# Optimization experiments

Measured on AMD Instinct MI355X. Metric: run time of the kernel, lower is better.

Reference implementation:

```python
import jax, jax.numpy as jnp
import numpy as np

B, CH, T = 8, 512, 1024
HEADS = 8
KC = CH // HEADS  # 64
BLOCK = 256       # block_length


def setup_inputs() -> dict:
    key = jax.random.key(0)
    ks = jax.random.split(key, 10)
    s = 0.05
    x = jax.random.normal(ks[0], (B, CH, T), jnp.float32)
    c = jax.random.normal(ks[1], (B, CH, T), jnp.float32)
    attn_mask = jnp.ones((1, 1, T, T), jnp.int32)
    # 1x1 Conv1d weights are just [out, in] matrices over the channel dim.
    Wq = jax.random.normal(ks[2], (CH, CH), jnp.float32) * s
    bq = jax.random.normal(ks[3], (CH,), jnp.float32) * s
    Wk = jax.random.normal(ks[4], (CH, CH), jnp.float32) * s
    bk = jax.random.normal(ks[5], (CH,), jnp.float32) * s
    Wv = jax.random.normal(ks[6], (CH, CH), jnp.float32) * s
    bv = jax.random.normal(ks[7], (CH,), jnp.float32) * s
    Wo = jax.random.normal(ks[8], (CH, CH), jnp.float32) * s
    bo = jax.random.normal(ks[9], (CH,), jnp.float32) * s
    return {"x": x, "c": c, "attn_mask": attn_mask,
            "Wq": Wq, "bq": bq, "Wk": Wk, "bk": bk,
            "Wv": Wv, "bv": bv, "Wo": Wo, "bo": bo}


def _proj(W, b, z):
    # 1x1 Conv1d: [B,C,T] -> [B,O,T]
    return jnp.einsum('oc,bct->bot', W, z) + b[None, :, None]


def reference(x, c, attn_mask, Wq, bq, Wk, bk, Wv, bv, Wo, bo):
    q = _proj(Wq, bq, x)
    k = _proj(Wk, bk, c)
    v = _proj(Wv, bv, c)

    def split_heads(z):  # [B,C,T] -> [B,H,T,KC]
        return z.reshape(B, HEADS, KC, T).transpose(0, 1, 3, 2)

    qh, kh, vh = split_heads(q), split_heads(k), split_heads(v)

    scale = jnp.asarray(1.0 / np.sqrt(KC), qh.dtype)
    scores = jnp.einsum('bhtd,bhsd->bhts', qh * scale, kh)  # [B,H,T,T]

    r = jnp.arange(T)
    diff = jnp.abs(r[None, :] - r[:, None])  # |i - j|, [T,T]
    # proximal bias: -log(1 + |i-j|)
    scores = scores + (-jnp.log1p(diff.astype(scores.dtype)))[None, None]
    # attention mask: masked_fill(mask == 0, -1e4)
    scores = jnp.where(attn_mask == 0, jnp.asarray(-1e4, scores.dtype), scores)
    # block-length band mask: keep |i-j| <= BLOCK (triu(-BLOCK).tril(BLOCK))
    band = (diff <= BLOCK)[None, None]
    scores = jnp.where(band, scores, jnp.asarray(-1e4, scores.dtype))

    p_attn = jax.nn.softmax(scores, axis=-1)
    out = jnp.einsum('bhts,bhsd->bhtd', p_attn, vh)  # [B,H,T,KC]
    out = out.transpose(0, 1, 3, 2).reshape(B, CH, T)  # merge heads -> [B,C,T]
    return _proj(Wo, bo, out)
```

## Files before the change

### kernel.cpp

```cpp
#include <hip/hip_runtime.h>
#include <stdint.h>

typedef unsigned short u16;
typedef __attribute__((ext_vector_type(8))) __bf16 bf16x8;
typedef __attribute__((ext_vector_type(4))) float f32x4;

constexpr int B_ = 8, CH = 512, T = 1024, NH = 8, HD = 64, BAND = 256;

__device__ inline u16 f2b(float f) {
  union { float f; uint32_t u; } v; v.f = f;
  uint32_t r = (v.u + 0x7fffu + ((v.u >> 16) & 1u)) >> 16;
  return (u16)r;
}

__device__ inline f32x4 mfma16(bf16x8 a, bf16x8 b, f32x4 c) {
  return __builtin_amdgcn_mfma_f32_16x16x32_bf16(a, b, c, 0, 0, 0);
}

__device__ __forceinline__ void gld16(const void* g, void* l) {
  __builtin_amdgcn_global_load_lds((__attribute__((address_space(1))) void*)(g),
                                   (__attribute__((address_space(3))) void*)(l),
                                   16, 0, 0);
}

__device__ __forceinline__ float exp2_hw(float x) { return __builtin_amdgcn_exp2f(x); }

__global__ __launch_bounds__(256) void cvt_w(const float* __restrict__ wq, const float* __restrict__ wk,
                                             const float* __restrict__ wv, const float* __restrict__ wo,
                                             u16* __restrict__ out) {
  int idx = blockIdx.x * 256 + threadIdx.x;
  int w = idx >> 15;
  const float* src = (w == 0) ? wq : (w == 1) ? wk : (w == 2) ? wv : wo;
  int e = (idx & 32767) * 8;
  f32x4 a = *(const f32x4*)(src + e);
  f32x4 b = *(const f32x4*)(src + e + 4);
  union { u16 h[8]; bf16x8 v; } r;
  r.h[0] = f2b(a[0]); r.h[1] = f2b(a[1]); r.h[2] = f2b(a[2]); r.h[3] = f2b(a[3]);
  r.h[4] = f2b(b[0]); r.h[5] = f2b(b[1]); r.h[6] = f2b(b[2]); r.h[7] = f2b(b[3]);
  *(bf16x8*)(out + (w << 18) + e) = r.v;
}

__global__ __launch_bounds__(256) void tr_cvt(const float* __restrict__ x, const float* __restrict__ c,
                                              u16* __restrict__ xT, u16* __restrict__ cT) {
  __shared__ float tile[32][33];
  int z = blockIdx.z;
  const float* src = (z < B_) ? x : c;
  u16* dst = (z < B_) ? xT : cT;
  int b = (z < B_) ? z : z - B_;
  int t0 = blockIdx.x * 32, c0 = blockIdx.y * 32;
  int tx = threadIdx.x & 31, ty = threadIdx.x >> 5;
#pragma unroll
  for (int k = 0; k < 4; k++)
    tile[ty + 8 * k][tx] = src[(long)(b * CH + c0 + ty + 8 * k) * T + t0 + tx];
  __syncthreads();
#pragma unroll
  for (int k = 0; k < 4; k++)
    dst[(long)(b * T + t0 + ty + 8 * k) * CH + c0 + tx] = f2b(tile[tx][ty + 8 * k]);
}

template <int TN, typename OT>
__device__ __forceinline__ void gemm_core(const u16* __restrict__ Ab, int lda,
                                          const u16* __restrict__ Bb, int ldb,
                                          OT* __restrict__ Cb, int ldc,
                                          const float* __restrict__ bi, bool brow,
                                          int m0, int n0, int K, u16* smA, u16* smB) {
  int t = threadIdx.x, lane = t & 63, wave = t >> 6;
  int cl = lane & 15, quad = lane >> 4;
  int wm = wave >> 1, wn = wave & 1;
  int rr = t >> 3, gs = t & 7;
  constexpr int NW = TN / 32;
  f32x4 acc[4][NW] = {};
  for (int k0 = 0; k0 < K; k0 += 64) {
    __syncthreads();
#pragma unroll
    for (int j = 0; j < 4; j++) {
      int R = j * 32 + rr;
      int gc = (gs ^ (R & 7)) << 3;
      gld16(Ab + (long)(m0 + R) * lda + k0 + gc, (char*)smA + j * 4096 + wave * 1024);
      if (j < TN / 32)
        gld16(Bb + (long)(n0 + R) * ldb + k0 + gc, (char*)smB + j * 4096 + wave * 1024);
    }
    __syncthreads();
#pragma unroll
    for (int ks = 0; ks < 2; ks++) {
      int g2 = ((ks << 2) | quad) ^ (cl & 7);
      bf16x8 af[4], bb[NW];
#pragma unroll
      for (int i = 0; i < 4; i++)
        af[i] = *(const bf16x8*)&smA[(wm * 64 + i * 16 + cl) * 64 + g2 * 8];
#pragma unroll
      for (int i = 0; i < NW; i++)
        bb[i] = *(const bf16x8*)&smB[(wn * (TN / 2) + i * 16 + cl) * 64 + g2 * 8];
#pragma unroll
      for (int mi = 0; mi < 4; mi++)
#pragma unroll
        for (int ni = 0; ni < NW; ni++)
          acc[mi][ni] = mfma16(af[mi], bb[ni], acc[mi][ni]);
    }
  }
#pragma unroll
  for (int mi = 0; mi < 4; mi++) {
    int row = m0 + wm * 64 + mi * 16 + quad * 4;
#pragma unroll
    for (int ni = 0; ni < NW; ni++) {
      int col = n0 + wn * (TN / 2) + ni * 16 + cl;
#pragma unroll
      for (int r = 0; r < 4; r++) {
        float v = acc[mi][ni][r] + (brow ? bi[row + r] : bi[col]);
        if constexpr (sizeof(OT) == 2) Cb[(long)(row + r) * ldc + col] = f2b(v);
        else Cb[(long)(row + r) * ldc + col] = v;
      }
    }
  }
}

__global__ __launch_bounds__(256, 3) void gemm_qkv(const u16* __restrict__ xT, const u16* __restrict__ cT,
                                                   const u16* __restrict__ Wb,
                                                   u16* __restrict__ Qb, u16* __restrict__ Kb, u16* __restrict__ Vb,
                                                   const float* __restrict__ bq, const float* __restrict__ bk,
                                                   const float* __restrict__ bv) {
  __shared__ u16 smA[128 * 64], smB[128 * 64];
  const long TCH = (long)T * CH;
  int z = blockIdx.z, sec = z >> 3, zz = z & 7, bx = blockIdx.x;
  const u16 *Ab, *Bb; u16* Cb; const float* bi;
  int m0, n0, ldc; bool brow;
  if (sec == 0) {
    Ab = xT + zz * TCH; Bb = Wb;           Cb = Qb + zz * TCH;        bi = bq;
    m0 = (bx >> 2) * 128; n0 = (bx & 3) * 128; ldc = CH; brow = false;
  } else if (sec == 1) {
    Ab = cT + zz * TCH; Bb = Wb + 262144;  Cb = Kb + zz * TCH;        bi = bk;
    m0 = (bx >> 2) * 128; n0 = (bx & 3) * 128; ldc = CH; brow = false;
  } else {
    Ab = Wb + 2 * 262144; Bb = cT + zz * TCH; Cb = Vb + zz * (long)CH * T; bi = bv;
    m0 = (bx & 3) * 128; n0 = (bx >> 2) * 128; ldc = T; brow = true;
  }
  gemm_core<128, u16>(Ab, CH, Bb, CH, Cb, ldc, bi, brow, m0, n0, CH, smA, smB);
}

__global__ __launch_bounds__(256, 4) void gemm_o(const u16* __restrict__ Wo, const u16* __restrict__ AO,
                                                 float* __restrict__ out, const float* __restrict__ bo) {
  __shared__ u16 smA[128 * 64], smB[64 * 64];
  int z = blockIdx.z;
  gemm_core<64, float>(Wo, CH, AO + z * (long)T * CH, CH, out + z * (long)CH * T, T,
                       bo, true, blockIdx.y * 128, blockIdx.x * 64, CH, smA, smB);
}

__global__ __launch_bounds__(256, 3) void attn(const u16* __restrict__ Q, const u16* __restrict__ Kt,
                                               const u16* __restrict__ V, u16* __restrict__ AO) {
  __shared__ u16 sK[2][64 * 64];
  __shared__ u16 sV[2][64 * 64];
  __shared__ u16 sP[4][16 * 72];
  int lane = threadIdx.x & 63, wave = threadIdx.x >> 6;
  int cl = lane & 15, quad = lane >> 4;
  int bx = blockIdx.x;
  int xcd = bx & 7, ii = bx >> 3;
  int bh = xcd * 8 + (ii & 7);
  int qt = ii >> 3;
  int b = bh >> 3, h = bh & 7;
  int tq0 = qt * 64;
  int tqw = tq0 + wave * 16;
  const u16* qb = Q + ((long)(b * T + tqw + cl) * CH) + h * HD;
  bf16x8 qf0 = *(const bf16x8*)(qb + quad * 8);
  bf16x8 qf1 = *(const bf16x8*)(qb + 32 + quad * 8);
  f32x4 acc[4] = {};
  float lr[4] = {0.f, 0.f, 0.f, 0.f};
  float fir[4];
#pragma unroll
  for (int r = 0; r < 4; r++) fir[r] = (float)(tqw + quad * 4 + r);
  int lo = tq0 - BAND; if (lo < 0) lo = 0;
  int hi = tq0 + 64 + BAND; if (hi > T) hi = T;
  int nt = (hi - lo) >> 6;

  int rl = lane >> 3, cg = lane & 7;
  const u16* ksrc = Kt + (long)b * T * CH + h * HD;
  const u16* vsrc = V + ((long)(b * CH + h * HD) * T);

#define STAGE(buf, j0)                                                          \
  {                                                                             \
    _Pragma("unroll")                                                           \
    for (int i = 0; i < 2; i++) {                                               \
      int r = wave * 16 + i * 8 + rl;                                           \
      int s = ((r >> 5) << 5) + ((r >> 4) & 1) + ((r & 15) << 1);               \
      gld16(ksrc + (long)(j0 + s) * CH + ((cg ^ (r & 7)) << 3),                 \
            (char*)&sK[buf][(wave * 16 + i * 8) * 64]);                         \
      gld16(vsrc + (long)r * T + (j0) + ((cg ^ (r & 7)) << 3),                  \
            (char*)&sV[buf][(wave * 16 + i * 8) * 64]);                         \
    }                                                                           \
  }

  STAGE(0, lo)
  constexpr float C2 = 0.125f * 1.4426950408889634f;
  for (int it = 0; it < nt; it++) {
    int cur = it & 1;
    int j0 = lo + it * 64;
    __syncthreads();
    if (it + 1 < nt) STAGE(1 - cur, j0 + 64)
    f32x4 sg[2][2];
#pragma unroll
    for (int p = 0; p < 2; p++)
#pragma unroll
      for (int sub = 0; sub < 2; sub++) {
        const u16* kr = &sK[cur][(p * 32 + sub * 16 + cl) * 64];
        bf16x8 k0 = *(const bf16x8*)&kr[((quad ^ (cl & 7)) << 3)];
        bf16x8 k1 = *(const bf16x8*)&kr[(((4 | quad) ^ (cl & 7)) << 3)];
        f32x4 z = {0.f, 0.f, 0.f, 0.f};
        sg[p][sub] = mfma16(qf1, k1, mfma16(qf0, k0, z));
      }
#pragma unroll
    for (int p = 0; p < 2; p++) {
      float jb = (float)(j0 + p * 32 + 2 * cl);
#pragma unroll
      for (int r = 0; r < 4; r++) {
        float de = fabsf(fir[r] - jb);
        float dd = fabsf(fir[r] - jb - 1.f);
        float pe = exp2_hw(sg[p][0][r] * C2) * __builtin_amdgcn_rcpf(1.f + de);
        float po = exp2_hw(sg[p][1][r] * C2) * __builtin_amdgcn_rcpf(1.f + dd);
        pe = (de <= 256.f) ? pe : 0.f;
        po = (dd <= 256.f) ? po : 0.f;
        lr[r] += pe + po;
        uint32_t ue, uo;
        { union { float f; uint32_t u; } cv; cv.f = pe; ue = cv.u; cv.f = po; uo = cv.u; }
        uint32_t pk = ((uo + 0x8000u) & 0xffff0000u) | ((ue + 0x8000u) >> 16);
        *(uint32_t*)&sP[wave][(quad * 4 + r) * 72 + p * 32 + 2 * cl] = pk;
      }
    }
#pragma unroll
    for (int ks = 0; ks < 2; ks++) {
      bf16x8 pf = *(bf16x8*)&sP[wave][cl * 72 + ks * 32 + quad * 8];
#pragma unroll
      for (int dg = 0; dg < 4; dg++) {
        bf16x8 vf = *(const bf16x8*)&sV[cur][(dg * 16 + cl) * 64 +
                                             ((((ks << 2) | quad) ^ (cl & 7)) << 3)];
        acc[dg] = mfma16(pf, vf, acc[dg]);
      }
    }
  }
#undef STAGE
  float inv[4];
#pragma unroll
  for (int r = 0; r < 4; r++) {
    float s = lr[r];
    s += __shfl_xor(s, 1); s += __shfl_xor(s, 2);
    s += __shfl_xor(s, 4); s += __shfl_xor(s, 8);
    inv[r] = __builtin_amdgcn_rcpf(s);
  }
#pragma unroll
  for (int dg = 0; dg < 4; dg++)
#pragma unroll
    for (int r = 0; r < 4; r++)
      AO[((long)(b * T + tqw + quad * 4 + r) * CH) + h * HD + dg * 16 + cl] = f2b(acc[dg][r] * inv[r]);
}

extern "C" void kernel_launch(void* const* d_in, const int* in_sizes, int n_in,
                              void* d_out, int out_size, void* d_ws, size_t ws_size,
                              hipStream_t stream) {
  const float* x  = (const float*)d_in[0];
  const float* c  = (const float*)d_in[1];
  const float* Wq = (const float*)d_in[3];
  const float* bq = (const float*)d_in[4];
  const float* Wk = (const float*)d_in[5];
  const float* bk = (const float*)d_in[6];
  const float* Wv = (const float*)d_in[7];
  const float* bv = (const float*)d_in[8];
  const float* Wo = (const float*)d_in[9];
  const float* bo = (const float*)d_in[10];
  float* out = (float*)d_out;

  const long NT = (long)B_ * T * CH;
  u16* Wb = (u16*)d_ws;
  u16* xT = Wb + 4 * 262144;
  u16* cT = xT + NT;
  u16* Qb = cT + NT;
  u16* Kb = Qb + NT;
  u16* Vb = Kb + NT;
  u16* AO = xT;

  cvt_w<<<dim3(512), dim3(256), 0, stream>>>(Wq, Wk, Wv, Wo, Wb);
  tr_cvt<<<dim3(32, 16, 16), dim3(256), 0, stream>>>(x, c, xT, cT);
  gemm_qkv<<<dim3(32, 1, 24), dim3(256), 0, stream>>>(xT, cT, Wb, Qb, Kb, Vb, bq, bk, bv);
  attn<<<dim3(1024), dim3(256), 0, stream>>>(Qb, Kb, Vb, AO);
  gemm_o<<<dim3(16, 4, 8), dim3(256), 0, stream>>>(Wb + 3 * 262144, AO, out, bo);
}
```

Before: 153.1 us.

## Double-buffer GEMM LDS loads and process two query tiles per attention block

The shared GEMM core now keeps two LDS buffers so the next K-slice is fetched while the current one is multiplied, with launch bounds lowered to fit the larger shared memory. The attention kernel now has each wave handle two 16-row query groups (128 queries per block) against the same staged K/V tiles, which halves the grid and reuses each K/V load for twice the queries. The cost is more registers and LDS per block and lower occupancy. The band window per block also widens, so some tiles fall entirely outside the band for one of the query groups and are computed anyway.

```diff
diff --git a/kernel.cpp b/kernel.cpp
--- a/kernel.cpp
+++ b/kernel.cpp
@@ -70,27 +70,36 @@
   int rr = t >> 3, gs = t & 7;
   constexpr int NW = TN / 32;
   f32x4 acc[4][NW] = {};
-  for (int k0 = 0; k0 < K; k0 += 64) {
-    __syncthreads();
+  auto stage = [&](int buf, int k0) {
 #pragma unroll
     for (int j = 0; j < 4; j++) {
       int R = j * 32 + rr;
       int gc = (gs ^ (R & 7)) << 3;
-      gld16(Ab + (long)(m0 + R) * lda + k0 + gc, (char*)smA + j * 4096 + wave * 1024);
-      if (j < TN / 32)
-        gld16(Bb + (long)(n0 + R) * ldb + k0 + gc, (char*)smB + j * 4096 + wave * 1024);
-    }
+      gld16(Ab + (long)(m0 + R) * lda + k0 + gc,
+            (char*)(smA + buf * 128 * 64) + j * 4096 + wave * 1024);
+      if (j < NW)
+        gld16(Bb + (long)(n0 + R) * ldb + k0 + gc,
+              (char*)(smB + buf * TN * 64) + j * 4096 + wave * 1024);
+    }
+  };
+  stage(0, 0);
+  int nk = K >> 6;
+  for (int it = 0; it < nk; it++) {
+    int cur = it & 1;
     __syncthreads();
+    if (it + 1 < nk) stage(1 - cur, (it + 1) << 6);
+    const u16* bA = smA + cur * 128 * 64;
+    const u16* bB = smB + cur * TN * 64;
 #pragma unroll
     for (int ks = 0; ks < 2; ks++) {
       int g2 = ((ks << 2) | quad) ^ (cl & 7);
       bf16x8 af[4], bb[NW];
 #pragma unroll
       for (int i = 0; i < 4; i++)
-        af[i] = *(const bf16x8*)&smA[(wm * 64 + i * 16 + cl) * 64 + g2 * 8];
+        af[i] = *(const bf16x8*)&bA[(wm * 64 + i * 16 + cl) * 64 + g2 * 8];
 #pragma unroll
       for (int i = 0; i < NW; i++)
-        bb[i] = *(const bf16x8*)&smB[(wn * (TN / 2) + i * 16 + cl) * 64 + g2 * 8];
+        bb[i] = *(const bf16x8*)&bB[(wn * (TN / 2) + i * 16 + cl) * 64 + g2 * 8];
 #pragma unroll
       for (int mi = 0; mi < 4; mi++)
 #pragma unroll
@@ -114,12 +123,12 @@
   }
 }
 
-__global__ __launch_bounds__(256, 3) void gemm_qkv(const u16* __restrict__ xT, const u16* __restrict__ cT,
+__global__ __launch_bounds__(256, 2) void gemm_qkv(const u16* __restrict__ xT, const u16* __restrict__ cT,
                                                    const u16* __restrict__ Wb,
                                                    u16* __restrict__ Qb, u16* __restrict__ Kb, u16* __restrict__ Vb,
                                                    const float* __restrict__ bq, const float* __restrict__ bk,
                                                    const float* __restrict__ bv) {
-  __shared__ u16 smA[128 * 64], smB[128 * 64];
+  __shared__ u16 smA[2 * 128 * 64], smB[2 * 128 * 64];
   const long TCH = (long)T * CH;
   int z = blockIdx.z, sec = z >> 3, zz = z & 7, bx = blockIdx.x;
   const u16 *Ab, *Bb; u16* Cb; const float* bi;
@@ -137,9 +146,9 @@
   gemm_core<128, u16>(Ab, CH, Bb, CH, Cb, ldc, bi, brow, m0, n0, CH, smA, smB);
 }
 
-__global__ __launch_bounds__(256, 4) void gemm_o(const u16* __restrict__ Wo, const u16* __restrict__ AO,
+__global__ __launch_bounds__(256, 3) void gemm_o(const u16* __restrict__ Wo, const u16* __restrict__ AO,
                                                  float* __restrict__ out, const float* __restrict__ bo) {
-  __shared__ u16 smA[128 * 64], smB[64 * 64];
+  __shared__ u16 smA[2 * 128 * 64], smB[2 * 64 * 64];
   int z = blockIdx.z;
   gemm_core<64, float>(Wo, CH, AO + z * (long)T * CH, CH, out + z * (long)CH * T, T,
                        bo, true, blockIdx.y * 128, blockIdx.x * 64, CH, smA, smB);
@@ -149,7 +158,7 @@
                                                const u16* __restrict__ V, u16* __restrict__ AO) {
   __shared__ u16 sK[2][64 * 64];
   __shared__ u16 sV[2][64 * 64];
-  __shared__ u16 sP[4][16 * 72];
+  __shared__ u16 sP[4][32 * 72];
   int lane = threadIdx.x & 63, wave = threadIdx.x >> 6;
   int cl = lane & 15, quad = lane >> 4;
   int bx = blockIdx.x;
@@ -157,18 +166,24 @@
   int bh = xcd * 8 + (ii & 7);
   int qt = ii >> 3;
   int b = bh >> 3, h = bh & 7;
-  int tq0 = qt * 64;
+  int tq0 = qt * 128;
   int tqw = tq0 + wave * 16;
-  const u16* qb = Q + ((long)(b * T + tqw + cl) * CH) + h * HD;
-  bf16x8 qf0 = *(const bf16x8*)(qb + quad * 8);
-  bf16x8 qf1 = *(const bf16x8*)(qb + 32 + quad * 8);
-  f32x4 acc[4] = {};
-  float lr[4] = {0.f, 0.f, 0.f, 0.f};
-  float fir[4];
-#pragma unroll
-  for (int r = 0; r < 4; r++) fir[r] = (float)(tqw + quad * 4 + r);
+  const u16* qb0 = Q + ((long)(b * T + tqw + cl) * CH) + h * HD;
+  const u16* qb1 = qb0 + (long)64 * CH;
+  bf16x8 qf[2][2];
+  qf[0][0] = *(const bf16x8*)(qb0 + quad * 8);
+  qf[0][1] = *(const bf16x8*)(qb0 + 32 + quad * 8);
+  qf[1][0] = *(const bf16x8*)(qb1 + quad * 8);
+  qf[1][1] = *(const bf16x8*)(qb1 + 32 + quad * 8);
+  f32x4 acc[2][4] = {};
+  float lr[2][4] = {};
+  float fir[2][4];
+#pragma unroll
+  for (int qg = 0; qg < 2; qg++)
+#pragma unroll
+    for (int r = 0; r < 4; r++) fir[qg][r] = (float)(tqw + qg * 64 + quad * 4 + r);
   int lo = tq0 - BAND; if (lo < 0) lo = 0;
-  int hi = tq0 + 64 + BAND; if (hi > T) hi = T;
+  int hi = tq0 + 128 + BAND; if (hi > T) hi = T;
   int nt = (hi - lo) >> 6;
 
   int rl = lane >> 3, cg = lane & 7;
@@ -195,7 +210,7 @@
     int j0 = lo + it * 64;
     __syncthreads();
     if (it + 1 < nt) STAGE(1 - cur, j0 + 64)
-    f32x4 sg[2][2];
+    f32x4 sg[2][2][2];
 #pragma unroll
     for (int p = 0; p < 2; p++)
 #pragma unroll
@@ -204,51 +219,60 @@
         bf16x8 k0 = *(const bf16x8*)&kr[((quad ^ (cl & 7)) << 3)];
         bf16x8 k1 = *(const bf16x8*)&kr[(((4 | quad) ^ (cl & 7)) << 3)];
         f32x4 z = {0.f, 0.f, 0.f, 0.f};
-        sg[p][sub] = mfma16(qf1, k1, mfma16(qf0, k0, z));
+        sg[0][p][sub] = mfma16(qf[0][1], k1, mfma16(qf[0][0], k0, z));
+        sg[1][p][sub] = mfma16(qf[1][1], k1, mfma16(qf[1][0], k0, z));
       }
 #pragma unroll
-    for (int p = 0; p < 2; p++) {
-      float jb = (float)(j0 + p * 32 + 2 * cl);
-#pragma unroll
-      for (int r = 0; r < 4; r++) {
-        float de = fabsf(fir[r] - jb);
-        float dd = fabsf(fir[r] - jb - 1.f);
-        float pe = exp2_hw(sg[p][0][r] * C2) * __builtin_amdgcn_rcpf(1.f + de);
-        float po = exp2_hw(sg[p][1][r] * C2) * __builtin_amdgcn_rcpf(1.f + dd);
-        pe = (de <= 256.f) ? pe : 0.f;
-        po = (dd <= 256.f) ? po : 0.f;
-        lr[r] += pe + po;
-        uint32_t ue, uo;
-        { union { float f; uint32_t u; } cv; cv.f = pe; ue = cv.u; cv.f = po; uo = cv.u; }
-        uint32_t pk = ((uo + 0x8000u) & 0xffff0000u) | ((ue + 0x8000u) >> 16);
-        *(uint32_t*)&sP[wave][(quad * 4 + r) * 72 + p * 32 + 2 * cl] = pk;
+    for (int qg = 0; qg < 2; qg++)
+#pragma unroll
+      for (int p = 0; p < 2; p++) {
+        float jb = (float)(j0 + p * 32 + 2 * cl);
+#pragma unroll
+        for (int r = 0; r < 4; r++) {
+          float de = fabsf(fir[qg][r] - jb);
+          float dd = fabsf(fir[qg][r] - jb - 1.f);
+          float pe = exp2_hw(sg[qg][p][0][r] * C2) * __builtin_amdgcn_rcpf(1.f + de);
+          float po = exp2_hw(sg[qg][p][1][r] * C2) * __builtin_amdgcn_rcpf(1.f + dd);
+          pe = (de <= 256.f) ? pe : 0.f;
+          po = (dd <= 256.f) ? po : 0.f;
+          lr[qg][r] += pe + po;
+          uint32_t ue, uo;
+          { union { float f; uint32_t u; } cv; cv.f = pe; ue = cv.u; cv.f = po; uo = cv.u; }
+          uint32_t pk = ((uo + 0x8000u) & 0xffff0000u) | ((ue + 0x8000u) >> 16);
+          *(uint32_t*)&sP[wave][(qg * 16 + quad * 4 + r) * 72 + p * 32 + 2 * cl] = pk;
+        }
       }
-    }
 #pragma unroll
     for (int ks = 0; ks < 2; ks++) {
-      bf16x8 pf = *(bf16x8*)&sP[wave][cl * 72 + ks * 32 + quad * 8];
+      bf16x8 pf0 = *(bf16x8*)&sP[wave][cl * 72 + ks * 32 + quad * 8];
+      bf16x8 pf1 = *(bf16x8*)&sP[wave][(16 + cl) * 72 + ks * 32 + quad * 8];
 #pragma unroll
       for (int dg = 0; dg < 4; dg++) {
         bf16x8 vf = *(const bf16x8*)&sV[cur][(dg * 16 + cl) * 64 +
                                              ((((ks << 2) | quad) ^ (cl & 7)) << 3)];
-        acc[dg] = mfma16(pf, vf, acc[dg]);
+        acc[0][dg] = mfma16(pf0, vf, acc[0][dg]);
+        acc[1][dg] = mfma16(pf1, vf, acc[1][dg]);
       }
     }
   }
 #undef STAGE
-  float inv[4];
-#pragma unroll
-  for (int r = 0; r < 4; r++) {
-    float s = lr[r];
-    s += __shfl_xor(s, 1); s += __shfl_xor(s, 2);
-    s += __shfl_xor(s, 4); s += __shfl_xor(s, 8);
-    inv[r] = __builtin_amdgcn_rcpf(s);
-  }
-#pragma unroll
-  for (int dg = 0; dg < 4; dg++)
-#pragma unroll
-    for (int r = 0; r < 4; r++)
-      AO[((long)(b * T + tqw + quad * 4 + r) * CH) + h * HD + dg * 16 + cl] = f2b(acc[dg][r] * inv[r]);
+#pragma unroll
+  for (int qg = 0; qg < 2; qg++) {
+    float inv[4];
+#pragma unroll
+    for (int r = 0; r < 4; r++) {
+      float s = lr[qg][r];
+      s += __shfl_xor(s, 1); s += __shfl_xor(s, 2);
+      s += __shfl_xor(s, 4); s += __shfl_xor(s, 8);
+      inv[r] = __builtin_amdgcn_rcpf(s);
+    }
+#pragma unroll
+    for (int dg = 0; dg < 4; dg++)
+#pragma unroll
+      for (int r = 0; r < 4; r++)
+        AO[((long)(b * T + tqw + qg * 64 + quad * 4 + r) * CH) + h * HD + dg * 16 + cl] =
+            f2b(acc[qg][dg][r] * inv[r]);
+  }
 }
 
 extern "C" void kernel_launch(void* const* d_in, const int* in_sizes, int n_in,
@@ -278,6 +302,6 @@
   cvt_w<<<dim3(512), dim3(256), 0, stream>>>(Wq, Wk, Wv, Wo, Wb);
   tr_cvt<<<dim3(32, 16, 16), dim3(256), 0, stream>>>(x, c, xT, cT);
   gemm_qkv<<<dim3(32, 1, 24), dim3(256), 0, stream>>>(xT, cT, Wb, Qb, Kb, Vb, bq, bk, bv);
-  attn<<<dim3(1024), dim3(256), 0, stream>>>(Qb, Kb, Vb, AO);
+  attn<<<dim3(512), dim3(256), 0, stream>>>(Qb, Kb, Vb, AO);
   gemm_o<<<dim3(16, 4, 8), dim3(256), 0, stream>>>(Wb + 3 * 262144, AO, out, bo);
 }
```

New measurement: 163.2 us. +6.6%, slower.
